# Optimization experiments

Hardware: AMD Instinct MI355X
Metric: run time of the kernel (lower is better)

Reference implementation:

```python
import jax, jax.numpy as jnp
import numpy as np

B, T, C = 1, 4096, 1024   # batch, seq, n_embd
E, K = 64, 8              # num_experts, router top-k
G, TG = 8, 4              # n_group, topk_group
H, HS = 512, 2048         # expert hidden, shared-expert hidden
STD = 0.02


def setup_inputs() -> dict:
    key = jax.random.key(0)
    ks = jax.random.split(key, 9)
    return {
        "x": jax.random.normal(ks[0], (B, T, C), jnp.float32),
        "router_w": jax.random.normal(ks[1], (E, C), jnp.float32) * (C ** -0.5),
        "e_bias": jnp.zeros((E,), jnp.float32),  # e_score_correction_bias buffer
        "gate_w": jax.random.normal(ks[2], (E, C, H), jnp.float32) * STD,
        "up_w": jax.random.normal(ks[3], (E, C, H), jnp.float32) * STD,
        "down_w": jax.random.normal(ks[4], (E, H, C), jnp.float32) * STD,
        "sh_gate_w": jax.random.normal(ks[5], (C, HS), jnp.float32) * STD,
        "sh_up_w": jax.random.normal(ks[6], (C, HS), jnp.float32) * STD,
        "sh_down_w": jax.random.normal(ks[7], (HS, C), jnp.float32) * STD,
    }


def _route(xf, router_w, e_bias):
    # grouped sigmoid top-k routing with score-correction bias (group_limited_greedy)
    S = xf.shape[0]
    scores = jax.nn.sigmoid(xf @ router_w.T)          # [S,E], raw sigmoid scores
    sb = scores + e_bias                               # biased scores (selection only)
    epg = E // G
    # per-group score = sum of top (K // topk_group) biased scores in that group
    grp = jax.lax.top_k(sb.reshape(S, G, epg), K // TG)[0].sum(-1)   # [S,G]
    gidx = jax.lax.top_k(grp, TG)[1]                                 # [S,TG]
    gmask = jnp.zeros((S, G), bool).at[jnp.arange(S)[:, None], gidx].set(True)
    emask = jnp.repeat(gmask, epg, axis=1)                           # [S,E]
    masked = jnp.where(emask, sb, -jnp.inf)
    topk_idx = jax.lax.top_k(masked, K)[1]                           # [S,K]
    w = jnp.take_along_axis(scores, topk_idx, axis=1)                # raw scores gathered
    w = w / (w.sum(-1, keepdims=True) + 1e-20)                       # norm_topk_prob
    return topk_idx, w


def reference(x, router_w, e_bias, gate_w, up_w, down_w, sh_gate_w, sh_up_w, sh_down_w):
    Bq, Tq, Cq = x.shape
    xf = x.reshape(Bq * Tq, Cq)
    # always-on shared expert (SwiGLU)
    shared = (jax.nn.silu(xf @ sh_gate_w) * (xf @ sh_up_w)) @ sh_down_w
    topk_idx, w = _route(xf, router_w, e_bias)
    fe = topk_idx.reshape(-1)                          # [S*K] expert id per routed row
    order = jnp.argsort(fe, stable=True)               # sort rows by expert (grouped)
    tok = order // K                                   # source token of each sorted row
    sorted_x = xf[tok]                                 # [S*K, C]
    group_sizes = jnp.bincount(fe, length=E).astype(jnp.int32)
    # grouped GEMMs (== torch._grouped_mm / bmm-over-buckets in the original)
    g = jax.lax.ragged_dot(sorted_x, gate_w, group_sizes)
    u = jax.lax.ragged_dot(sorted_x, up_w, group_sizes)
    h = jax.nn.silu(g) * u
    o = jax.lax.ragged_dot(h, down_w, group_sizes)     # [S*K, C]
    o = o * w.reshape(-1)[order][:, None]              # weight by routing prob
    routed = jnp.zeros_like(xf).at[tok].add(o)         # combine back per token
    return (shared + routed).reshape(Bq, Tq, Cq)
```

## Files before the change

kernel.cpp:

```cpp
#include <hip/hip_runtime.h>
#include <hip/hip_bf16.h>
#include <stdint.h>


#define S_TOK 4096
#define C_DIM 1024
#define E_NUM 64
#define H_DIM 512
#define HS_DIM 2048
#define ROWS_TOTAL (S_TOK * 8)
#define T_TILES 320
#define NB_ROUTED_F (T_TILES * 8)
#define NB_SHARED_F (32 * 32)
#define NB_ROUTED_D (T_TILES * 8)
#define NB_SHARED_D (32 * 8)
#define NB_SCATTER  (ROWS_TOTAL / 256)

typedef __attribute__((ext_vector_type(8))) short short8;
typedef __attribute__((ext_vector_type(4))) float f32x4;
typedef __attribute__((ext_vector_type(2))) unsigned int uint2v;

static __device__ __forceinline__ unsigned short f2bf(float f) {
    union { float f; uint32_t u; } v; v.f = f;
    uint32_t u = v.u;
    u += 0x7fffu + ((u >> 16) & 1u);
    return (unsigned short)(u >> 16);
}

static __device__ __forceinline__ uint32_t cvtpk(float a, float b) {
    uint32_t r;
    asm("v_cvt_pk_bf16_f32 %0, %1, %2" : "=v"(r) : "v"(a), "v"(b));
    return r;
}

static __device__ __forceinline__ void gl2lds16(const void* g, void* l) {
    __builtin_amdgcn_global_load_lds(
        (const __attribute__((address_space(1))) uint32_t*)g,
        (__attribute__((address_space(3))) uint32_t*)l, 16, 0, 0);
}

__global__ __launch_bounds__(256)
void router_topk_k(const float* __restrict__ x, const float* __restrict__ rw,
                   const float* __restrict__ ebias,
                   int* __restrict__ topk_idx, float* __restrict__ topk_w,
                   int* __restrict__ counts, int* __restrict__ done,
                   int* __restrict__ base, int* __restrict__ cursor,
                   int* __restrict__ tile_e, int* __restrict__ tile_m0) {
    int t0 = blockIdx.x * 32;
    __shared__ float xs[32][36];
    __shared__ float wsm[64][36];
    __shared__ float scf[32][64];
    __shared__ int last_blk;
    int t = threadIdx.x;
    int tx = t & 15, ty = t >> 4;
    float acc[2][4] = {};
    for (int k0 = 0; k0 < C_DIM; k0 += 32) {
        {
            int r = t >> 3, c = t & 7;
            *(float4*)&xs[r][c * 4] = *(const float4*)(x + (size_t)(t0 + r) * C_DIM + k0 + c * 4);
        }
        #pragma unroll
        for (int i = 0; i < 2; i++) {
            int idx = t + 256 * i;
            int r = idx >> 3, c = idx & 7;
            *(float4*)&wsm[r][c * 4] = *(const float4*)(rw + (size_t)r * C_DIM + k0 + c * 4);
        }
        __syncthreads();
        #pragma unroll
        for (int kk = 0; kk < 32; kk += 4) {
            float4 a0 = *(const float4*)&xs[ty * 2 + 0][kk];
            float4 a1 = *(const float4*)&xs[ty * 2 + 1][kk];
            #pragma unroll
            for (int j = 0; j < 4; j++) {
                float4 b = *(const float4*)&wsm[tx * 4 + j][kk];
                acc[0][j] += a0.x * b.x + a0.y * b.y + a0.z * b.z + a0.w * b.w;
                acc[1][j] += a1.x * b.x + a1.y * b.y + a1.z * b.z + a1.w * b.w;
            }
        }
        __syncthreads();
    }
    #pragma unroll
    for (int i = 0; i < 2; i++)
        #pragma unroll
        for (int j = 0; j < 4; j++)
            scf[ty * 2 + i][tx * 4 + j] = 1.f / (1.f + __expf(-acc[i][j]));
    __syncthreads();

    int lane = t & 63, w = t >> 6;
    float eb = ebias[lane];
    for (int r = 0; r < 8; r++) {
        int lt = w * 8 + r;
        int tok = t0 + lt;
        float sc = scf[lt][lane];
        float sb = sc + eb;
        float m1 = sb, m2 = -1e30f;
        #pragma unroll
        for (int off = 1; off <= 4; off <<= 1) {
            float o1 = __shfl_xor(m1, off);
            float o2 = __shfl_xor(m2, off);
            float hi = fmaxf(m1, o1), lo = fminf(m1, o1);
            m2 = fmaxf(lo, fmaxf(m2, o2));
            m1 = hi;
        }
        float grp = m1 + m2;
        float grpv[8];
        #pragma unroll
        for (int g = 0; g < 8; g++) grpv[g] = __shfl(grp, g * 8);
        unsigned gsel = 0;
        #pragma unroll
        for (int k = 0; k < 4; k++) {
            float best = -1e30f; int bi = 0;
            #pragma unroll
            for (int g = 0; g < 8; g++)
                if (!((gsel >> g) & 1) && grpv[g] > best) { best = grpv[g]; bi = g; }
            gsel |= 1u << bi;
        }
        float val = ((gsel >> (lane >> 3)) & 1) ? sb : -1e30f;
        int idx[8]; float sv[8]; float wsum = 0.f;
        #pragma unroll
        for (int k = 0; k < 8; k++) {
            uint32_t u = __float_as_uint(val);
            uint32_t mu = (u & 0x80000000u) ? ~u : (u | 0x80000000u);
            unsigned long long key = ((unsigned long long)mu << 6) | (unsigned long long)(63 - lane);
            #pragma unroll
            for (int off = 32; off; off >>= 1) {
                unsigned long long ok = __shfl_xor(key, off);
                if (ok > key) key = ok;
            }
            int win = 63 - (int)(key & 63ull);
            idx[k] = win;
            sv[k] = __shfl(sc, win);
            wsum += sv[k];
            if (lane == win) val = -1e30f;
        }
        float inv = 1.f / (wsum + 1e-20f);
        if (lane < 8) {
            topk_idx[tok * 8 + lane] = idx[lane];
            topk_w[tok * 8 + lane] = sv[lane] * inv;
            atomicAdd(&counts[idx[lane]], 1);
        }
    }

    __threadfence();
    __syncthreads();
    if (t == 0) last_blk = (atomicAdd(done, 1) == (int)gridDim.x - 1) ? 1 : 0;
    __syncthreads();
    if (last_blk && t < 64) {
        __threadfence();
        int e = t;
        int c = atomicAdd(&counts[e], 0);
        int s = c;
        #pragma unroll
        for (int off = 1; off < 64; off <<= 1) {
            int o = __shfl_up(s, off);
            if (e >= off) s += o;
        }
        int ex = s - c;
        base[e] = ex;
        cursor[e] = ex;
        int nt = (c + 127) >> 7;
        int ts = nt;
        #pragma unroll
        for (int off = 1; off < 64; off <<= 1) {
            int o = __shfl_up(ts, off);
            if (e >= off) ts += o;
        }
        int tb = ts - nt;
        for (int i = 0; i < nt; i++) { tile_e[tb + i] = e; tile_m0[tb + i] = i * 128; }
        int total = __shfl(ts, 63);
        for (int j = total + e; j < T_TILES; j += 64) tile_e[j] = -1;
    }
}

__global__ __launch_bounds__(256)
void scatter_xcvt_k(const int* __restrict__ topk_idx, const float* __restrict__ topk_w,
                    int* __restrict__ cursor, int* __restrict__ row_token,
                    float* __restrict__ row_wgt, int* __restrict__ pos_of,
                    const float* __restrict__ x, unsigned short* __restrict__ xb) {
    int bid = blockIdx.x;
    if (bid < NB_SCATTER) {
        int i = bid * 256 + threadIdx.x;
        int e = topk_idx[i];
        int pos = atomicAdd(&cursor[e], 1);
        row_token[pos] = i >> 3;
        row_wgt[pos] = topk_w[i];
        pos_of[i] = pos;
        return;
    }
    int g = (bid - NB_SCATTER) * 256 + threadIdx.x;
    float4 v0 = ((const float4*)x)[4 * g];
    float4 v1 = ((const float4*)x)[4 * g + 1];
    float4 v2 = ((const float4*)x)[4 * g + 2];
    float4 v3 = ((const float4*)x)[4 * g + 3];
    uint32_t pk[8];
    pk[0] = cvtpk(v0.x, v0.y); pk[1] = cvtpk(v0.z, v0.w);
    pk[2] = cvtpk(v1.x, v1.y); pk[3] = cvtpk(v1.z, v1.w);
    pk[4] = cvtpk(v2.x, v2.y); pk[5] = cvtpk(v2.z, v2.w);
    pk[6] = cvtpk(v3.x, v3.y); pk[7] = cvtpk(v3.z, v3.w);
    ((uint4*)xb)[2 * g]     = *(uint4*)&pk[0];
    ((uint4*)xb)[2 * g + 1] = *(uint4*)&pk[4];
}

__global__ __launch_bounds__(256)
void combine_k(const float* __restrict__ O, const int* __restrict__ pos_of,
               float* __restrict__ out) {
    int t = blockIdx.x;
    int c = threadIdx.x;
    float4 s = ((const float4*)(out + (size_t)t * C_DIM))[c];
    int p[8];
    #pragma unroll
    for (int k = 0; k < 8; k++) p[k] = pos_of[t * 8 + k];
    #pragma unroll
    for (int k = 0; k < 8; k++) {
        float4 v = ((const float4*)(O + (size_t)p[k] * C_DIM))[c];
        s.x += v.x; s.y += v.y; s.z += v.z; s.w += v.w;
    }
    ((float4*)(out + (size_t)t * C_DIM))[c] = s;
}

__global__ __launch_bounds__(256, 3)
void fused_all_k(const short* __restrict__ xb,
                 const float* __restrict__ gate_w, const float* __restrict__ up_w,
                 const float* __restrict__ shg_w, const float* __restrict__ shu_w,
                 unsigned short* __restrict__ Hr, unsigned short* __restrict__ Hs,
                 const int* __restrict__ counts, const int* __restrict__ base,
                 const int* __restrict__ row_token,
                 const int* __restrict__ tile_e, const int* __restrict__ tile_m0) {
    constexpr int K = C_DIM;

    int bid = blockIdx.x;
    bool routed = bid < NB_ROUTED_F;
    const float* B1; const float* B2; unsigned short* Cout;
    int m0, n0, Mrows, rowbase, N;
    if (routed) {
        int ti = bid >> 3;
        int e = tile_e[ti];
        if (e < 0) return;
        m0 = tile_m0[ti]; n0 = (bid & 7) * 64;
        Mrows = counts[e]; rowbase = base[e];
        N = H_DIM;
        B1 = gate_w + (size_t)e * K * H_DIM;
        B2 = up_w   + (size_t)e * K * H_DIM;
        Cout = Hr;
    } else {
        int s = bid - NB_ROUTED_F;
        m0 = (s >> 5) * 128; n0 = (s & 31) * 64;
        Mrows = S_TOK; rowbase = 0;
        N = HS_DIM;
        B1 = shg_w; B2 = shu_w;
        Cout = Hs;
    }

    __shared__ short As[3 * 4096];
    __shared__ short Bs1[2 * 2048];
    __shared__ short Bs2[2 * 2048];

    int tid = threadIdx.x;
    int lane = tid & 63, w = tid >> 6;
    int wr = w >> 1, wc = w & 1;
    int quad = lane >> 4, l16 = lane & 15;
    int sr = lane >> 2, sc = lane & 3;

    const short* aptr[2];
    #pragma unroll
    for (int i = 0; i < 2; i++) {
        int row = w * 32 + i * 16 + sr;
        int mrow = m0 + row;
        int cl = mrow < Mrows ? mrow : (Mrows - 1);
        size_t arow = routed ? (size_t)row_token[rowbase + cl] : (size_t)cl;
        aptr[i] = xb + arow * K + sc * 8;
    }

    int nb = tid & 63, kg = tid >> 6;
    const float* b1g = B1 + (size_t)(kg * 8) * N + n0 + nb;
    const float* b2g = B2 + (size_t)(kg * 8) * N + n0 + nb;
    const int bwr = nb * 32 + ((kg * 8) ^ ((nb & 3) << 3));

    f32x4 acc1[4][2] = {};
    f32x4 acc2[4][2] = {};

    const int nk = K >> 5;
    auto stageA = [&](int slot) {
        #pragma unroll
        for (int i = 0; i < 2; i++) {
            gl2lds16(aptr[i], &As[slot * 4096 + (w * 32 + i * 16) * 32]);
            aptr[i] += 32;
        }
    };
    auto loadB = [&](float (&fb)[2][8]) {
        #pragma unroll
        for (int jj = 0; jj < 8; jj++) fb[0][jj] = b1g[(size_t)jj * N];
        #pragma unroll
        for (int jj = 0; jj < 8; jj++) fb[1][jj] = b2g[(size_t)jj * N];
        b1g += (size_t)32 * N;
        b2g += (size_t)32 * N;
    };
    auto writeB = [&](int buf, float (&fb)[2][8]) {
        uint32_t w0[4], w1[4];
        #pragma unroll
        for (int q = 0; q < 4; q++) {
            w0[q] = cvtpk(fb[0][2 * q], fb[0][2 * q + 1]);
            w1[q] = cvtpk(fb[1][2 * q], fb[1][2 * q + 1]);
        }
        *(uint4*)&Bs1[buf * 2048 + bwr] = *(uint4*)w0;
        *(uint4*)&Bs2[buf * 2048 + bwr] = *(uint4*)w1;
    };

    float fbA[2][8], fbB[2][8];
    stageA(0);
    stageA(1);
    __builtin_amdgcn_sched_barrier(0);
    {
        float fb0[2][8];
        loadB(fb0);
        writeB(0, fb0);
    }
    __builtin_amdgcn_sched_barrier(0);
    loadB(fbA);
    asm volatile("s_waitcnt vmcnt(16) lgkmcnt(0)" ::: "memory");
    __builtin_amdgcn_s_barrier();
    __builtin_amdgcn_sched_barrier(0);

    auto kstep = [&](int t, float (&fbIn)[2][8], float (&fbOut)[2][8]) {
        int slot = t % 3;
        int bbuf = t & 1;
        bool pf = (t + 2 < nk);
        if (pf) { stageA((t + 2) % 3); loadB(fbOut); }

        short8 a[4], b1[2], b2[2];
        #pragma unroll
        for (int i = 0; i < 4; i++)
            a[i] = *(const short8*)&As[slot * 4096 + (wr * 64 + i * 16 + l16) * 32 + quad * 8];
        #pragma unroll
        for (int j = 0; j < 2; j++) {
            int row = wc * 32 + j * 16 + l16;
            int ro = row * 32 + ((quad * 8) ^ ((row & 3) << 3));
            b1[j] = *(const short8*)&Bs1[bbuf * 2048 + ro];
            b2[j] = *(const short8*)&Bs2[bbuf * 2048 + ro];
        }
        #pragma unroll
        for (int i = 0; i < 4; i++)
            #pragma unroll
            for (int j = 0; j < 2; j++) {
                acc1[i][j] = __builtin_amdgcn_mfma_f32_16x16x32_bf16(a[i], b1[j], acc1[i][j], 0, 0, 0);
                acc2[i][j] = __builtin_amdgcn_mfma_f32_16x16x32_bf16(a[i], b2[j], acc2[i][j], 0, 0, 0);
            }
        if (t + 1 < nk) {
            writeB((t + 1) & 1, fbIn);
            if (pf) asm volatile("s_waitcnt vmcnt(18) lgkmcnt(0)" ::: "memory");
            else    asm volatile("s_waitcnt vmcnt(0) lgkmcnt(0)" ::: "memory");
            __builtin_amdgcn_s_barrier();
            __builtin_amdgcn_sched_barrier(0);
        }
    };

    for (int t = 0; t < nk; t += 2) {
        kstep(t, fbA, fbB);
        if (t + 1 < nk) kstep(t + 1, fbB, fbA);
    }

    #pragma unroll
    for (int i = 0; i < 4; i++) {
        #pragma unroll
        for (int rr = 0; rr < 4; rr++) {
            int row = m0 + wr * 64 + i * 16 + quad * 4 + rr;
            if (row >= Mrows) continue;
            size_t orow = (size_t)(rowbase + row);
            #pragma unroll
            for (int j = 0; j < 2; j++) {
                int n = n0 + wc * 32 + j * 16 + l16;
                float v = acc1[i][j][rr];
                float u = acc2[i][j][rr];
                float h = v / (1.f + __expf(-v)) * u;
                Cout[orow * N + n] = f2bf(h);
            }
        }
    }
}

__global__ __launch_bounds__(256, 3)
void down_all_k(const short* __restrict__ Hr, const short* __restrict__ Hs,
                const float* __restrict__ down_w, const float* __restrict__ shd_w,
                float* __restrict__ O, float* __restrict__ out,
                const int* __restrict__ counts, const int* __restrict__ base,
                const float* __restrict__ row_wgt,
                const int* __restrict__ tile_e, const int* __restrict__ tile_m0) {
    constexpr int N = C_DIM;

    int bid = blockIdx.x;
    bool shared_e = bid < NB_SHARED_D;
    const short* A; const float* B1; float* Cout;
    int m0, n0, Mrows, rowbase, K;
    if (shared_e) {
        m0 = (bid >> 3) * 128; n0 = (bid & 7) * 128;
        Mrows = S_TOK; rowbase = 0;
        K = HS_DIM;
        A = Hs;
        B1 = shd_w;
        Cout = out;
    } else {
        int rb = bid - NB_SHARED_D;
        int ti = rb >> 3;
        int e = tile_e[ti];
        if (e < 0) return;
        m0 = tile_m0[ti]; n0 = (rb & 7) * 128;
        Mrows = counts[e]; rowbase = base[e];
        K = H_DIM;
        A = Hr;
        B1 = down_w + (size_t)e * H_DIM * N;
        Cout = O;
    }

    __shared__ short As[3 * 4096];
    __shared__ short Bs1[2 * 4096];

    int tid = threadIdx.x;
    int lane = tid & 63, w = tid >> 6;
    int wr = w >> 1, wc = w & 1;
    int quad = lane >> 4, l16 = lane & 15;
    int sr = lane >> 2, sc = lane & 3;

    const short* aptr[2];
    #pragma unroll
    for (int i = 0; i < 2; i++) {
        int row = w * 32 + i * 16 + sr;
        int mrow = m0 + row;
        int cl = mrow < Mrows ? mrow : (Mrows - 1);
        aptr[i] = A + (size_t)(rowbase + cl) * K + sc * 8;
    }

    int nb = tid & 63, kg = tid >> 6;
    const float* b1g = B1 + (size_t)(kg * 8) * N + n0 + nb;
    const int bwr = nb * 32 + ((kg * 8) ^ ((nb & 3) << 3));

    f32x4 acc1[4][4] = {};

    const int nk = K >> 5;
    auto stageA = [&](int slot) {
        #pragma unroll
        for (int i = 0; i < 2; i++) {
            gl2lds16(aptr[i], &As[slot * 4096 + (w * 32 + i * 16) * 32]);
            aptr[i] += 32;
        }
    };
    auto loadB = [&](float (&fb)[2][8]) {
        #pragma unroll
        for (int jj = 0; jj < 8; jj++) fb[0][jj] = b1g[(size_t)jj * N];
        #pragma unroll
        for (int jj = 0; jj < 8; jj++) fb[1][jj] = b1g[(size_t)jj * N + 64];
        b1g += (size_t)32 * N;
    };
    auto writeB = [&](int buf, float (&fb)[2][8]) {
        uint32_t w0[4], w1[4];
        #pragma unroll
        for (int q = 0; q < 4; q++) {
            w0[q] = cvtpk(fb[0][2 * q], fb[0][2 * q + 1]);
            w1[q] = cvtpk(fb[1][2 * q], fb[1][2 * q + 1]);
        }
        *(uint4*)&Bs1[buf * 4096 + bwr] = *(uint4*)w0;
        *(uint4*)&Bs1[buf * 4096 + bwr + 64 * 32] = *(uint4*)w1;
    };

    float fbA[2][8], fbB[2][8];
    stageA(0);
    stageA(1);
    __builtin_amdgcn_sched_barrier(0);
    {
        float fb0[2][8];
        loadB(fb0);
        writeB(0, fb0);
    }
    __builtin_amdgcn_sched_barrier(0);
    loadB(fbA);
    asm volatile("s_waitcnt vmcnt(16) lgkmcnt(0)" ::: "memory");
    __builtin_amdgcn_s_barrier();
    __builtin_amdgcn_sched_barrier(0);

    auto kstep = [&](int t, float (&fbIn)[2][8], float (&fbOut)[2][8]) {
        int slot = t % 3;
        int bbuf = t & 1;
        bool pf = (t + 2 < nk);
        if (pf) { stageA((t + 2) % 3); loadB(fbOut); }

        short8 a[4], b1[4];
        #pragma unroll
        for (int i = 0; i < 4; i++)
            a[i] = *(const short8*)&As[slot * 4096 + (wr * 64 + i * 16 + l16) * 32 + quad * 8];
        #pragma unroll
        for (int j = 0; j < 4; j++) {
            int row = wc * 64 + j * 16 + l16;
            int ro = row * 32 + ((quad * 8) ^ ((row & 3) << 3));
            b1[j] = *(const short8*)&Bs1[bbuf * 4096 + ro];
        }
        #pragma unroll
        for (int i = 0; i < 4; i++)
            #pragma unroll
            for (int j = 0; j < 4; j++)
                acc1[i][j] = __builtin_amdgcn_mfma_f32_16x16x32_bf16(a[i], b1[j], acc1[i][j], 0, 0, 0);
        if (t + 1 < nk) {
            writeB((t + 1) & 1, fbIn);
            if (pf) asm volatile("s_waitcnt vmcnt(18) lgkmcnt(0)" ::: "memory");
            else    asm volatile("s_waitcnt vmcnt(0) lgkmcnt(0)" ::: "memory");
            __builtin_amdgcn_s_barrier();
            __builtin_amdgcn_sched_barrier(0);
        }
    };

    for (int t = 0; t < nk; t += 2) {
        kstep(t, fbA, fbB);
        if (t + 1 < nk) kstep(t + 1, fbB, fbA);
    }

    #pragma unroll
    for (int i = 0; i < 4; i++) {
        #pragma unroll
        for (int rr = 0; rr < 4; rr++) {
            int row = m0 + wr * 64 + i * 16 + quad * 4 + rr;
            if (row >= Mrows) continue;
            size_t orow = (size_t)(rowbase + row);
            float scl = shared_e ? 1.f : row_wgt[rowbase + row];
            #pragma unroll
            for (int j = 0; j < 4; j++) {
                int n = n0 + wc * 64 + j * 16 + l16;
                Cout[orow * N + n] = acc1[i][j][rr] * scl;
            }
        }
    }
}

extern "C" void kernel_launch(void* const* d_in, const int* in_sizes, int n_in,
                              void* d_out, int out_size, void* d_ws, size_t ws_size,
                              hipStream_t stream) {
    const float* x        = (const float*)d_in[0];
    const float* router_w = (const float*)d_in[1];
    const float* e_bias   = (const float*)d_in[2];
    const float* gate_w   = (const float*)d_in[3];
    const float* up_w     = (const float*)d_in[4];
    const float* down_w   = (const float*)d_in[5];
    const float* sh_gate  = (const float*)d_in[6];
    const float* sh_up    = (const float*)d_in[7];
    const float* sh_down  = (const float*)d_in[8];
    float* out = (float*)d_out;
    char* ws = (char*)d_ws;

    int*   counts    = (int*)(ws);
    int*   base      = (int*)(ws + 256);
    int*   cursor    = (int*)(ws + 512);
    int*   done      = (int*)(ws + 768);
    int*   topk_idx  = (int*)(ws + 1024);
    float* topk_w    = (float*)(ws + 1024 + 131072);
    int*   row_token = (int*)(ws + 1024 + 2 * 131072);
    float* row_wgt   = (float*)(ws + 1024 + 3 * 131072);
    int*   pos_of    = (int*)(ws + 1664 * 1024);
    int*   tile_e    = (int*)(ws + 1800 * 1024);
    int*   tile_m0   = (int*)(ws + 1808 * 1024);
    const size_t MB = 1u << 20;
    unsigned short* xb = (unsigned short*)(ws + 2 * MB);
    unsigned short* Hs = (unsigned short*)(ws + 10 * MB);
    unsigned short* Hr = (unsigned short*)(ws + 26 * MB);
    float*          O  = (float*)(ws + 70 * MB);

    hipMemsetAsync(ws, 0, 1024, stream);

    router_topk_k<<<S_TOK / 32, 256, 0, stream>>>(
        x, router_w, e_bias, topk_idx, topk_w, counts, done,
        base, cursor, tile_e, tile_m0);

    const int NX = S_TOK * C_DIM / 16;
    scatter_xcvt_k<<<NB_SCATTER + NX / 256, 256, 0, stream>>>(
        topk_idx, topk_w, cursor, row_token, row_wgt, pos_of, x, xb);

    fused_all_k<<<NB_ROUTED_F + NB_SHARED_F, 256, 0, stream>>>(
        (const short*)xb, gate_w, up_w, sh_gate, sh_up, Hr, Hs,
        counts, base, row_token, tile_e, tile_m0);

    down_all_k<<<NB_SHARED_D + NB_ROUTED_D, 256, 0, stream>>>(
        (const short*)Hr, (const short*)Hs, down_w, sh_down,
        O, out, counts, base, row_wgt, tile_e, tile_m0);

    combine_k<<<S_TOK, 256, 0, stream>>>(O, pos_of, out);
}
```

Before: 829.0 us.

## Fuse scatter and bf16 conversion into router kernel; vectorize B-tile loads

Merges the scatter and x-to-bf16 conversion kernel into the router kernel. Each block converts its 32 tokens' rows, then spins on a global flag set by the last block (after the prefix scan) before scattering its own routed rows. This removes one launch and overlaps the conversion with the wait for routing. The GEMM B-tile loaders now use float2 loads covering two adjacent columns, with a matching LDS swizzle and adjusted vmcnt waits, cutting the number of global load instructions. The spin-wait assumes all 128 blocks are co-resident, which holds at this grid size.

```diff
diff --git a/kernel.cpp b/kernel.cpp
--- a/kernel.cpp
+++ b/kernel.cpp
@@ -14,7 +14,6 @@
 #define NB_SHARED_F (32 * 32)
 #define NB_ROUTED_D (T_TILES * 8)
 #define NB_SHARED_D (32 * 8)
-#define NB_SCATTER  (ROWS_TOTAL / 256)
 
 typedef __attribute__((ext_vector_type(8))) short short8;
 typedef __attribute__((ext_vector_type(4))) float f32x4;
@@ -40,12 +39,14 @@
 }
 
 __global__ __launch_bounds__(256)
-void router_topk_k(const float* __restrict__ x, const float* __restrict__ rw,
-                   const float* __restrict__ ebias,
-                   int* __restrict__ topk_idx, float* __restrict__ topk_w,
-                   int* __restrict__ counts, int* __restrict__ done,
-                   int* __restrict__ base, int* __restrict__ cursor,
-                   int* __restrict__ tile_e, int* __restrict__ tile_m0) {
+void router_all_k(const float* __restrict__ x, const float* __restrict__ rw,
+                  const float* __restrict__ ebias,
+                  int* __restrict__ topk_idx, float* __restrict__ topk_w,
+                  int* __restrict__ counts, int* __restrict__ done, int* __restrict__ flag,
+                  int* __restrict__ base, int* __restrict__ cursor,
+                  int* __restrict__ tile_e, int* __restrict__ tile_m0,
+                  int* __restrict__ row_token, float* __restrict__ row_wgt,
+                  int* __restrict__ pos_of, unsigned short* __restrict__ xb) {
     int t0 = blockIdx.x * 32;
     __shared__ float xs[32][36];
     __shared__ float wsm[64][36];
@@ -145,60 +146,66 @@
     __syncthreads();
     if (t == 0) last_blk = (atomicAdd(done, 1) == (int)gridDim.x - 1) ? 1 : 0;
     __syncthreads();
-    if (last_blk && t < 64) {
+
+    if (last_blk) {
+        if (t < 64) {
+            int e = t;
+            int c = atomicAdd(&counts[e], 0);
+            int s = c;
+            #pragma unroll
+            for (int off = 1; off < 64; off <<= 1) {
+                int o = __shfl_up(s, off);
+                if (e >= off) s += o;
+            }
+            int ex = s - c;
+            base[e] = ex;
+            cursor[e] = ex;
+            int nt = (c + 127) >> 7;
+            int ts = nt;
+            #pragma unroll
+            for (int off = 1; off < 64; off <<= 1) {
+                int o = __shfl_up(ts, off);
+                if (e >= off) ts += o;
+            }
+            int tb = ts - nt;
+            for (int i = 0; i < nt; i++) { tile_e[tb + i] = e; tile_m0[tb + i] = i * 128; }
+            int total = __shfl(ts, 63);
+            for (int j = total + e; j < T_TILES; j += 64) tile_e[j] = -1;
+        }
+        __syncthreads();
         __threadfence();
-        int e = t;
-        int c = atomicAdd(&counts[e], 0);
-        int s = c;
-        #pragma unroll
-        for (int off = 1; off < 64; off <<= 1) {
-            int o = __shfl_up(s, off);
-            if (e >= off) s += o;
-        }
-        int ex = s - c;
-        base[e] = ex;
-        cursor[e] = ex;
-        int nt = (c + 127) >> 7;
-        int ts = nt;
-        #pragma unroll
-        for (int off = 1; off < 64; off <<= 1) {
-            int o = __shfl_up(ts, off);
-            if (e >= off) ts += o;
-        }
-        int tb = ts - nt;
-        for (int i = 0; i < nt; i++) { tile_e[tb + i] = e; tile_m0[tb + i] = i * 128; }
-        int total = __shfl(ts, 63);
-        for (int j = total + e; j < T_TILES; j += 64) tile_e[j] = -1;
-    }
-}
-
-__global__ __launch_bounds__(256)
-void scatter_xcvt_k(const int* __restrict__ topk_idx, const float* __restrict__ topk_w,
-                    int* __restrict__ cursor, int* __restrict__ row_token,
-                    float* __restrict__ row_wgt, int* __restrict__ pos_of,
-                    const float* __restrict__ x, unsigned short* __restrict__ xb) {
-    int bid = blockIdx.x;
-    if (bid < NB_SCATTER) {
-        int i = bid * 256 + threadIdx.x;
+        if (t == 0) atomicExch(flag, 1);
+    }
+
+    #pragma unroll
+    for (int it = 0; it < 8; it++) {
+        int g = t0 * 64 + it * 256 + t;
+        float4 v0 = ((const float4*)x)[4 * g];
+        float4 v1 = ((const float4*)x)[4 * g + 1];
+        float4 v2 = ((const float4*)x)[4 * g + 2];
+        float4 v3 = ((const float4*)x)[4 * g + 3];
+        uint32_t pk[8];
+        pk[0] = cvtpk(v0.x, v0.y); pk[1] = cvtpk(v0.z, v0.w);
+        pk[2] = cvtpk(v1.x, v1.y); pk[3] = cvtpk(v1.z, v1.w);
+        pk[4] = cvtpk(v2.x, v2.y); pk[5] = cvtpk(v2.z, v2.w);
+        pk[6] = cvtpk(v3.x, v3.y); pk[7] = cvtpk(v3.z, v3.w);
+        ((uint4*)xb)[2 * g]     = *(uint4*)&pk[0];
+        ((uint4*)xb)[2 * g + 1] = *(uint4*)&pk[4];
+    }
+
+    if (t == 0) {
+        while (atomicAdd(flag, 0) == 0) __builtin_amdgcn_s_sleep(2);
+    }
+    __syncthreads();
+
+    {
+        int i = t0 * 8 + t;
         int e = topk_idx[i];
         int pos = atomicAdd(&cursor[e], 1);
         row_token[pos] = i >> 3;
         row_wgt[pos] = topk_w[i];
         pos_of[i] = pos;
-        return;
-    }
-    int g = (bid - NB_SCATTER) * 256 + threadIdx.x;
-    float4 v0 = ((const float4*)x)[4 * g];
-    float4 v1 = ((const float4*)x)[4 * g + 1];
-    float4 v2 = ((const float4*)x)[4 * g + 2];
-    float4 v3 = ((const float4*)x)[4 * g + 3];
-    uint32_t pk[8];
-    pk[0] = cvtpk(v0.x, v0.y); pk[1] = cvtpk(v0.z, v0.w);
-    pk[2] = cvtpk(v1.x, v1.y); pk[3] = cvtpk(v1.z, v1.w);
-    pk[4] = cvtpk(v2.x, v2.y); pk[5] = cvtpk(v2.z, v2.w);
-    pk[6] = cvtpk(v3.x, v3.y); pk[7] = cvtpk(v3.z, v3.w);
-    ((uint4*)xb)[2 * g]     = *(uint4*)&pk[0];
-    ((uint4*)xb)[2 * g + 1] = *(uint4*)&pk[4];
+    }
 }
 
 __global__ __launch_bounds__(256)
@@ -271,10 +278,11 @@
         aptr[i] = xb + arow * K + sc * 8;
     }
 
-    int nb = tid & 63, kg = tid >> 6;
-    const float* b1g = B1 + (size_t)(kg * 8) * N + n0 + nb;
-    const float* b2g = B2 + (size_t)(kg * 8) * N + n0 + nb;
-    const int bwr = nb * 32 + ((kg * 8) ^ ((nb & 3) << 3));
+    int nb2 = tid & 31, kg2 = tid >> 5;
+    const float* b1g = B1 + (size_t)(kg2 * 4) * N + n0 + nb2 * 2;
+    const float* b2g = B2 + (size_t)(kg2 * 4) * N + n0 + nb2 * 2;
+    const int bmask = (nb2 & 3) << 3;
+    const int bw0 = (nb2 * 2) * 32 + ((kg2 * 4) ^ bmask);
 
     f32x4 acc1[4][2] = {};
     f32x4 acc2[4][2] = {};
@@ -287,41 +295,42 @@
             aptr[i] += 32;
         }
     };
-    auto loadB = [&](float (&fb)[2][8]) {
-        #pragma unroll
-        for (int jj = 0; jj < 8; jj++) fb[0][jj] = b1g[(size_t)jj * N];
-        #pragma unroll
-        for (int jj = 0; jj < 8; jj++) fb[1][jj] = b2g[(size_t)jj * N];
+    auto loadB = [&](float2 (&fb)[2][4]) {
+        #pragma unroll
+        for (int j = 0; j < 4; j++) fb[0][j] = *(const float2*)(b1g + (size_t)j * N);
+        #pragma unroll
+        for (int j = 0; j < 4; j++) fb[1][j] = *(const float2*)(b2g + (size_t)j * N);
         b1g += (size_t)32 * N;
         b2g += (size_t)32 * N;
     };
-    auto writeB = [&](int buf, float (&fb)[2][8]) {
-        uint32_t w0[4], w1[4];
-        #pragma unroll
-        for (int q = 0; q < 4; q++) {
-            w0[q] = cvtpk(fb[0][2 * q], fb[0][2 * q + 1]);
-            w1[q] = cvtpk(fb[1][2 * q], fb[1][2 * q + 1]);
-        }
-        *(uint4*)&Bs1[buf * 2048 + bwr] = *(uint4*)w0;
-        *(uint4*)&Bs2[buf * 2048 + bwr] = *(uint4*)w1;
-    };
-
-    float fbA[2][8], fbB[2][8];
+    auto writeB = [&](int buf, float2 (&fb)[2][4]) {
+        uint2v v;
+        v[0] = cvtpk(fb[0][0].x, fb[0][1].x); v[1] = cvtpk(fb[0][2].x, fb[0][3].x);
+        *(uint2v*)&Bs1[buf * 2048 + bw0] = v;
+        v[0] = cvtpk(fb[0][0].y, fb[0][1].y); v[1] = cvtpk(fb[0][2].y, fb[0][3].y);
+        *(uint2v*)&Bs1[buf * 2048 + bw0 + 32] = v;
+        v[0] = cvtpk(fb[1][0].x, fb[1][1].x); v[1] = cvtpk(fb[1][2].x, fb[1][3].x);
+        *(uint2v*)&Bs2[buf * 2048 + bw0] = v;
+        v[0] = cvtpk(fb[1][0].y, fb[1][1].y); v[1] = cvtpk(fb[1][2].y, fb[1][3].y);
+        *(uint2v*)&Bs2[buf * 2048 + bw0 + 32] = v;
+    };
+
+    float2 fbA[2][4], fbB[2][4];
     stageA(0);
     stageA(1);
     __builtin_amdgcn_sched_barrier(0);
     {
-        float fb0[2][8];
+        float2 fb0[2][4];
         loadB(fb0);
         writeB(0, fb0);
     }
     __builtin_amdgcn_sched_barrier(0);
     loadB(fbA);
-    asm volatile("s_waitcnt vmcnt(16) lgkmcnt(0)" ::: "memory");
+    asm volatile("s_waitcnt vmcnt(8) lgkmcnt(0)" ::: "memory");
     __builtin_amdgcn_s_barrier();
     __builtin_amdgcn_sched_barrier(0);
 
-    auto kstep = [&](int t, float (&fbIn)[2][8], float (&fbOut)[2][8]) {
+    auto kstep = [&](int t, float2 (&fbIn)[2][4], float2 (&fbOut)[2][4]) {
         int slot = t % 3;
         int bbuf = t & 1;
         bool pf = (t + 2 < nk);
@@ -334,7 +343,7 @@
         #pragma unroll
         for (int j = 0; j < 2; j++) {
             int row = wc * 32 + j * 16 + l16;
-            int ro = row * 32 + ((quad * 8) ^ ((row & 3) << 3));
+            int ro = row * 32 + ((quad * 8) ^ (((row >> 1) & 3) << 3));
             b1[j] = *(const short8*)&Bs1[bbuf * 2048 + ro];
             b2[j] = *(const short8*)&Bs2[bbuf * 2048 + ro];
         }
@@ -347,7 +356,7 @@
             }
         if (t + 1 < nk) {
             writeB((t + 1) & 1, fbIn);
-            if (pf) asm volatile("s_waitcnt vmcnt(18) lgkmcnt(0)" ::: "memory");
+            if (pf) asm volatile("s_waitcnt vmcnt(10) lgkmcnt(0)" ::: "memory");
             else    asm volatile("s_waitcnt vmcnt(0) lgkmcnt(0)" ::: "memory");
             __builtin_amdgcn_s_barrier();
             __builtin_amdgcn_sched_barrier(0);
@@ -429,9 +438,12 @@
         aptr[i] = A + (size_t)(rowbase + cl) * K + sc * 8;
     }
 
-    int nb = tid & 63, kg = tid >> 6;
-    const float* b1g = B1 + (size_t)(kg * 8) * N + n0 + nb;
-    const int bwr = nb * 32 + ((kg * 8) ^ ((nb & 3) << 3));
+    int nb2 = tid & 63, kg2 = tid >> 6;
+    const float* b1g = B1 + (size_t)(kg2 * 8) * N + n0 + nb2 * 2;
+    const int bmask = (nb2 & 3) << 3;
+    const int bc0 = (nb2 * 2) * 32;
+    const int bo0 = (kg2 * 8) ^ bmask;
+    const int bo1 = (kg2 * 8 + 4) ^ bmask;
 
     f32x4 acc1[4][4] = {};
 
@@ -443,40 +455,39 @@
             aptr[i] += 32;
         }
     };
-    auto loadB = [&](float (&fb)[2][8]) {
-        #pragma unroll
-        for (int jj = 0; jj < 8; jj++) fb[0][jj] = b1g[(size_t)jj * N];
-        #pragma unroll
-        for (int jj = 0; jj < 8; jj++) fb[1][jj] = b1g[(size_t)jj * N + 64];
+    auto loadB = [&](float2 (&fb)[8]) {
+        #pragma unroll
+        for (int j = 0; j < 8; j++) fb[j] = *(const float2*)(b1g + (size_t)j * N);
         b1g += (size_t)32 * N;
     };
-    auto writeB = [&](int buf, float (&fb)[2][8]) {
-        uint32_t w0[4], w1[4];
-        #pragma unroll
-        for (int q = 0; q < 4; q++) {
-            w0[q] = cvtpk(fb[0][2 * q], fb[0][2 * q + 1]);
-            w1[q] = cvtpk(fb[1][2 * q], fb[1][2 * q + 1]);
-        }
-        *(uint4*)&Bs1[buf * 4096 + bwr] = *(uint4*)w0;
-        *(uint4*)&Bs1[buf * 4096 + bwr + 64 * 32] = *(uint4*)w1;
-    };
-
-    float fbA[2][8], fbB[2][8];
+    auto writeB = [&](int buf, float2 (&fb)[8]) {
+        uint2v v;
+        v[0] = cvtpk(fb[0].x, fb[1].x); v[1] = cvtpk(fb[2].x, fb[3].x);
+        *(uint2v*)&Bs1[buf * 4096 + bc0 + bo0] = v;
+        v[0] = cvtpk(fb[4].x, fb[5].x); v[1] = cvtpk(fb[6].x, fb[7].x);
+        *(uint2v*)&Bs1[buf * 4096 + bc0 + bo1] = v;
+        v[0] = cvtpk(fb[0].y, fb[1].y); v[1] = cvtpk(fb[2].y, fb[3].y);
+        *(uint2v*)&Bs1[buf * 4096 + bc0 + 32 + bo0] = v;
+        v[0] = cvtpk(fb[4].y, fb[5].y); v[1] = cvtpk(fb[6].y, fb[7].y);
+        *(uint2v*)&Bs1[buf * 4096 + bc0 + 32 + bo1] = v;
+    };
+
+    float2 fbA[8], fbB[8];
     stageA(0);
     stageA(1);
     __builtin_amdgcn_sched_barrier(0);
     {
-        float fb0[2][8];
+        float2 fb0[8];
         loadB(fb0);
         writeB(0, fb0);
     }
     __builtin_amdgcn_sched_barrier(0);
     loadB(fbA);
-    asm volatile("s_waitcnt vmcnt(16) lgkmcnt(0)" ::: "memory");
+    asm volatile("s_waitcnt vmcnt(8) lgkmcnt(0)" ::: "memory");
     __builtin_amdgcn_s_barrier();
     __builtin_amdgcn_sched_barrier(0);
 
-    auto kstep = [&](int t, float (&fbIn)[2][8], float (&fbOut)[2][8]) {
+    auto kstep = [&](int t, float2 (&fbIn)[8], float2 (&fbOut)[8]) {
         int slot = t % 3;
         int bbuf = t & 1;
         bool pf = (t + 2 < nk);
@@ -489,7 +500,7 @@
         #pragma unroll
         for (int j = 0; j < 4; j++) {
             int row = wc * 64 + j * 16 + l16;
-            int ro = row * 32 + ((quad * 8) ^ ((row & 3) << 3));
+            int ro = row * 32 + ((quad * 8) ^ (((row >> 1) & 3) << 3));
             b1[j] = *(const short8*)&Bs1[bbuf * 4096 + ro];
         }
         #pragma unroll
@@ -499,7 +510,7 @@
                 acc1[i][j] = __builtin_amdgcn_mfma_f32_16x16x32_bf16(a[i], b1[j], acc1[i][j], 0, 0, 0);
         if (t + 1 < nk) {
             writeB((t + 1) & 1, fbIn);
-            if (pf) asm volatile("s_waitcnt vmcnt(18) lgkmcnt(0)" ::: "memory");
+            if (pf) asm volatile("s_waitcnt vmcnt(10) lgkmcnt(0)" ::: "memory");
             else    asm volatile("s_waitcnt vmcnt(0) lgkmcnt(0)" ::: "memory");
             __builtin_amdgcn_s_barrier();
             __builtin_amdgcn_sched_barrier(0);
@@ -547,6 +558,7 @@
     int*   base      = (int*)(ws + 256);
     int*   cursor    = (int*)(ws + 512);
     int*   done      = (int*)(ws + 768);
+    int*   flag      = (int*)(ws + 772);
     int*   topk_idx  = (int*)(ws + 1024);
     float* topk_w    = (float*)(ws + 1024 + 131072);
     int*   row_token = (int*)(ws + 1024 + 2 * 131072);
@@ -562,13 +574,9 @@
 
     hipMemsetAsync(ws, 0, 1024, stream);
 
-    router_topk_k<<<S_TOK / 32, 256, 0, stream>>>(
-        x, router_w, e_bias, topk_idx, topk_w, counts, done,
-        base, cursor, tile_e, tile_m0);
-
-    const int NX = S_TOK * C_DIM / 16;
-    scatter_xcvt_k<<<NB_SCATTER + NX / 256, 256, 0, stream>>>(
-        topk_idx, topk_w, cursor, row_token, row_wgt, pos_of, x, xb);
+    router_all_k<<<S_TOK / 32, 256, 0, stream>>>(
+        x, router_w, e_bias, topk_idx, topk_w, counts, done, flag,
+        base, cursor, tile_e, tile_m0, row_token, row_wgt, pos_of, xb);
 
     fused_all_k<<<NB_ROUTED_F + NB_SHARED_F, 256, 0, stream>>>(
         (const short*)xb, gate_w, up_w, sh_gate, sh_up, Hr, Hs,
```

New measurement: 868.1 us. 1.05x slower.

## Fuse scatter and bf16 conversion into router kernel with grid-wide flag spin

Applied to the files above, without the earlier changes.

Merges the scatter and x-to-bf16 conversion kernel into the router kernel. Each of the 128 blocks converts its own 32 token rows to bf16, then spins on a global flag set by the last block once it has computed the expert prefix sums, and then scatters its own routed rows. This removes one kernel launch and its inter-kernel gap. It relies on all 128 blocks being co-resident for the spin-wait to avoid deadlock, which holds for this grid size.

```diff
diff --git a/kernel.cpp b/kernel.cpp
--- a/kernel.cpp
+++ b/kernel.cpp
@@ -14,7 +14,6 @@
 #define NB_SHARED_F (32 * 32)
 #define NB_ROUTED_D (T_TILES * 8)
 #define NB_SHARED_D (32 * 8)
-#define NB_SCATTER  (ROWS_TOTAL / 256)
 
 typedef __attribute__((ext_vector_type(8))) short short8;
 typedef __attribute__((ext_vector_type(4))) float f32x4;
@@ -40,12 +39,14 @@
 }
 
 __global__ __launch_bounds__(256)
-void router_topk_k(const float* __restrict__ x, const float* __restrict__ rw,
-                   const float* __restrict__ ebias,
-                   int* __restrict__ topk_idx, float* __restrict__ topk_w,
-                   int* __restrict__ counts, int* __restrict__ done,
-                   int* __restrict__ base, int* __restrict__ cursor,
-                   int* __restrict__ tile_e, int* __restrict__ tile_m0) {
+void router_all_k(const float* __restrict__ x, const float* __restrict__ rw,
+                  const float* __restrict__ ebias,
+                  int* __restrict__ topk_idx, float* __restrict__ topk_w,
+                  int* __restrict__ counts, int* __restrict__ done, int* __restrict__ flag,
+                  int* __restrict__ base, int* __restrict__ cursor,
+                  int* __restrict__ tile_e, int* __restrict__ tile_m0,
+                  int* __restrict__ row_token, float* __restrict__ row_wgt,
+                  int* __restrict__ pos_of, unsigned short* __restrict__ xb) {
     int t0 = blockIdx.x * 32;
     __shared__ float xs[32][36];
     __shared__ float wsm[64][36];
@@ -145,60 +146,66 @@
     __syncthreads();
     if (t == 0) last_blk = (atomicAdd(done, 1) == (int)gridDim.x - 1) ? 1 : 0;
     __syncthreads();
-    if (last_blk && t < 64) {
+
+    if (last_blk) {
+        if (t < 64) {
+            int e = t;
+            int c = atomicAdd(&counts[e], 0);
+            int s = c;
+            #pragma unroll
+            for (int off = 1; off < 64; off <<= 1) {
+                int o = __shfl_up(s, off);
+                if (e >= off) s += o;
+            }
+            int ex = s - c;
+            base[e] = ex;
+            cursor[e] = ex;
+            int nt = (c + 127) >> 7;
+            int ts = nt;
+            #pragma unroll
+            for (int off = 1; off < 64; off <<= 1) {
+                int o = __shfl_up(ts, off);
+                if (e >= off) ts += o;
+            }
+            int tb = ts - nt;
+            for (int i = 0; i < nt; i++) { tile_e[tb + i] = e; tile_m0[tb + i] = i * 128; }
+            int total = __shfl(ts, 63);
+            for (int j = total + e; j < T_TILES; j += 64) tile_e[j] = -1;
+        }
+        __syncthreads();
         __threadfence();
-        int e = t;
-        int c = atomicAdd(&counts[e], 0);
-        int s = c;
-        #pragma unroll
-        for (int off = 1; off < 64; off <<= 1) {
-            int o = __shfl_up(s, off);
-            if (e >= off) s += o;
-        }
-        int ex = s - c;
-        base[e] = ex;
-        cursor[e] = ex;
-        int nt = (c + 127) >> 7;
-        int ts = nt;
-        #pragma unroll
-        for (int off = 1; off < 64; off <<= 1) {
-            int o = __shfl_up(ts, off);
-            if (e >= off) ts += o;
-        }
-        int tb = ts - nt;
-        for (int i = 0; i < nt; i++) { tile_e[tb + i] = e; tile_m0[tb + i] = i * 128; }
-        int total = __shfl(ts, 63);
-        for (int j = total + e; j < T_TILES; j += 64) tile_e[j] = -1;
-    }
-}
-
-__global__ __launch_bounds__(256)
-void scatter_xcvt_k(const int* __restrict__ topk_idx, const float* __restrict__ topk_w,
-                    int* __restrict__ cursor, int* __restrict__ row_token,
-                    float* __restrict__ row_wgt, int* __restrict__ pos_of,
-                    const float* __restrict__ x, unsigned short* __restrict__ xb) {
-    int bid = blockIdx.x;
-    if (bid < NB_SCATTER) {
-        int i = bid * 256 + threadIdx.x;
+        if (t == 0) atomicExch(flag, 1);
+    }
+
+    #pragma unroll
+    for (int it = 0; it < 8; it++) {
+        int g = t0 * 64 + it * 256 + t;
+        float4 v0 = ((const float4*)x)[4 * g];
+        float4 v1 = ((const float4*)x)[4 * g + 1];
+        float4 v2 = ((const float4*)x)[4 * g + 2];
+        float4 v3 = ((const float4*)x)[4 * g + 3];
+        uint32_t pk[8];
+        pk[0] = cvtpk(v0.x, v0.y); pk[1] = cvtpk(v0.z, v0.w);
+        pk[2] = cvtpk(v1.x, v1.y); pk[3] = cvtpk(v1.z, v1.w);
+        pk[4] = cvtpk(v2.x, v2.y); pk[5] = cvtpk(v2.z, v2.w);
+        pk[6] = cvtpk(v3.x, v3.y); pk[7] = cvtpk(v3.z, v3.w);
+        ((uint4*)xb)[2 * g]     = *(uint4*)&pk[0];
+        ((uint4*)xb)[2 * g + 1] = *(uint4*)&pk[4];
+    }
+
+    if (t == 0) {
+        while (atomicAdd(flag, 0) == 0) __builtin_amdgcn_s_sleep(2);
+    }
+    __syncthreads();
+
+    {
+        int i = t0 * 8 + t;
         int e = topk_idx[i];
         int pos = atomicAdd(&cursor[e], 1);
         row_token[pos] = i >> 3;
         row_wgt[pos] = topk_w[i];
         pos_of[i] = pos;
-        return;
-    }
-    int g = (bid - NB_SCATTER) * 256 + threadIdx.x;
-    float4 v0 = ((const float4*)x)[4 * g];
-    float4 v1 = ((const float4*)x)[4 * g + 1];
-    float4 v2 = ((const float4*)x)[4 * g + 2];
-    float4 v3 = ((const float4*)x)[4 * g + 3];
-    uint32_t pk[8];
-    pk[0] = cvtpk(v0.x, v0.y); pk[1] = cvtpk(v0.z, v0.w);
-    pk[2] = cvtpk(v1.x, v1.y); pk[3] = cvtpk(v1.z, v1.w);
-    pk[4] = cvtpk(v2.x, v2.y); pk[5] = cvtpk(v2.z, v2.w);
-    pk[6] = cvtpk(v3.x, v3.y); pk[7] = cvtpk(v3.z, v3.w);
-    ((uint4*)xb)[2 * g]     = *(uint4*)&pk[0];
-    ((uint4*)xb)[2 * g + 1] = *(uint4*)&pk[4];
+    }
 }
 
 __global__ __launch_bounds__(256)
@@ -547,6 +554,7 @@
     int*   base      = (int*)(ws + 256);
     int*   cursor    = (int*)(ws + 512);
     int*   done      = (int*)(ws + 768);
+    int*   flag      = (int*)(ws + 772);
     int*   topk_idx  = (int*)(ws + 1024);
     float* topk_w    = (float*)(ws + 1024 + 131072);
     int*   row_token = (int*)(ws + 1024 + 2 * 131072);
@@ -562,13 +570,9 @@
 
     hipMemsetAsync(ws, 0, 1024, stream);
 
-    router_topk_k<<<S_TOK / 32, 256, 0, stream>>>(
-        x, router_w, e_bias, topk_idx, topk_w, counts, done,
-        base, cursor, tile_e, tile_m0);
-
-    const int NX = S_TOK * C_DIM / 16;
-    scatter_xcvt_k<<<NB_SCATTER + NX / 256, 256, 0, stream>>>(
-        topk_idx, topk_w, cursor, row_token, row_wgt, pos_of, x, xb);
+    router_all_k<<<S_TOK / 32, 256, 0, stream>>>(
+        x, router_w, e_bias, topk_idx, topk_w, counts, done, flag,
+        base, cursor, tile_e, tile_m0, row_token, row_wgt, pos_of, xb);
 
     fused_all_k<<<NB_ROUTED_F + NB_SHARED_F, 256, 0, stream>>>(
         (const short*)xb, gate_w, up_w, sh_gate, sh_up, Hr, Hs,
```

Result: no change. 826.6 us (median of 2 runs) (-0.3%).
